# Kernel optimization log

Hardware: AMD Instinct MI355X
Metric: run time of the kernel (lower is better)

Reference implementation:

```python
import jax, jax.numpy as jnp
import numpy as np

K, D, E = 2048, 128, 64

def setup_inputs() -> dict:
    key = jax.random.key(0)
    k1, k2, k3 = jax.random.split(key, 3)
    z = jax.random.normal(k1, (K, D), dtype=jnp.float32)
    # Kaiming-like scaling so logits stay in a sane range
    W1 = jax.random.normal(k2, (2 * D, E), dtype=jnp.float32) / jnp.sqrt(2.0 * D)
    b1 = jnp.zeros((E,), dtype=jnp.float32)
    W2 = jax.random.normal(k3, (E, 1), dtype=jnp.float32) / jnp.sqrt(1.0 * E)
    b2 = jnp.zeros((1,), dtype=jnp.float32)
    return {"z": z, "W1": W1, "b1": b1, "W2": W2, "b2": b2}


def reference(z, W1, b1, W2, b2):
    # edge_mlp(cat([z_i, z_j])) == z_i @ W1[:d] + z_j @ W1[d:] + b1  (avoids (k,k,2d) concat)
    d = z.shape[1]
    hi = z @ W1[:d]          # (k, e)  -- contribution of z_i (row/query)
    hj = z @ W1[d:]          # (k, e)  -- contribution of z_j (col/key)
    h = jax.nn.silu(hi[:, None, :] + hj[None, :, :] + b1)   # (k, k, e)
    logits = jnp.einsum('ije,eo->ij', h, W2) + b2[0]         # (k, k)
    return jax.nn.softmax(logits, axis=-1)
```

## Files before the change

kernel.cpp:

```cpp
#include <hip/hip_runtime.h>
#include <cstdint>
#include <cstddef>

#define KTOT 2048
#define DDIM 128
#define EDIM 64
#define RPB  2
#define KPB  4

#define LOG2E 1.44269504088896f

typedef float v2f __attribute__((ext_vector_type(2)));

__global__ void proj_kernel(const float* __restrict__ z,
                            const float* __restrict__ W1,
                            const float* __restrict__ b1,
                            float* __restrict__ hi,
                            float* __restrict__ hj) {
  __shared__ float zrow[KPB][DDIM];
  const int t  = threadIdx.x;
  const int k0 = blockIdx.x * KPB;
#pragma unroll
  for (int r = 0; r < KPB; ++r) zrow[r][t] = z[(size_t)(k0 + r) * DDIM + t];
  __syncthreads();

  const int  e    = t & 63;
  const bool isHj = (t >= 64);
  const float* Wcol = W1 + (isHj ? DDIM * EDIM : 0) + e;

  float acc[KPB];
  const float binit = isHj ? 0.0f : b1[e];
#pragma unroll
  for (int r = 0; r < KPB; ++r) acc[r] = binit;

#pragma unroll 4
  for (int d = 0; d < DDIM; ++d) {
    const float w = Wcol[(size_t)d * EDIM];
#pragma unroll
    for (int r = 0; r < KPB; ++r) acc[r] = fmaf(zrow[r][d], w, acc[r]);
  }

  float* dst = isHj ? hj : hi;
#pragma unroll
  for (int r = 0; r < KPB; ++r)
    dst[(size_t)(k0 + r) * EDIM + e] = acc[r] * LOG2E;
}

__device__ __forceinline__ float quad_term(float4 hiq, float4 hvq, float4 w2q) {
  const v2f t01 = (v2f){hiq.x, hiq.y} + (v2f){hvq.x, hvq.y};
  const v2f t23 = (v2f){hiq.z, hiq.w} + (v2f){hvq.z, hvq.w};
  const float e0 = __builtin_amdgcn_exp2f(-t01.x);
  const float e1 = __builtin_amdgcn_exp2f(-t01.y);
  const float e2 = __builtin_amdgcn_exp2f(-t23.x);
  const float e3 = __builtin_amdgcn_exp2f(-t23.y);
  const v2f d01 = (v2f){e0, e1} + 1.0f;
  const v2f d23 = (v2f){e2, e3} + 1.0f;
  const v2f u01 = t01 * (v2f){w2q.x, w2q.y};
  const v2f u23 = t23 * (v2f){w2q.z, w2q.w};
  const float p01 = d01.x * d01.y;
  const float p23 = d23.x * d23.y;
  const float rD  = __builtin_amdgcn_rcpf(p01 * p23);
  const float n01 = fmaf(u01.y, d01.x, u01.x * d01.y);
  const float n23 = fmaf(u23.y, d23.x, u23.x * d23.y);
  const float N   = fmaf(n23, p01, n01 * p23);
  return N * rD;
}

__global__ __launch_bounds__(512, 8) void edge_softmax_kernel(
    const float* __restrict__ hi, const float* __restrict__ hj,
    const float* __restrict__ w2, float* __restrict__ out) {
  __shared__ float logits[RPB][KTOT];
  __shared__ float ps[RPB][4];

  const int tid  = threadIdx.x;
  const int lane = tid & 63;
  const int wave = tid >> 6;
  const int sub  = lane & 7;
  const int jg   = lane >> 3;
  const int i0   = blockIdx.x * RPB;

  const float4 w2a = *reinterpret_cast<const float4*>(w2 + sub * 8);
  const float4 w2b = *reinterpret_cast<const float4*>(w2 + sub * 8 + 4);
  float4 hia[RPB], hib[RPB];
#pragma unroll
  for (int r = 0; r < RPB; ++r) {
    hia[r] = *reinterpret_cast<const float4*>(hi + (size_t)(i0 + r) * EDIM + sub * 8);
    hib[r] = *reinterpret_cast<const float4*>(hi + (size_t)(i0 + r) * EDIM + sub * 8 + 4);
  }

  const int jbase = wave * 8 + jg;
  const float* hjp = hj + (size_t)jbase * EDIM + sub * 8;

  float4 hva = *reinterpret_cast<const float4*>(hjp);
  float4 hvb = *reinterpret_cast<const float4*>(hjp + 4);

  for (int it = 0; it < KTOT / 64; ++it) {
    const float4 ca = hva, cb = hvb;
    if (it + 1 < KTOT / 64) {
      const float* p = hjp + (size_t)(it + 1) * 64 * EDIM;
      hva = *reinterpret_cast<const float4*>(p);
      hvb = *reinterpret_cast<const float4*>(p + 4);
    }
    const int j = jbase + it * 64;
#pragma unroll
    for (int r = 0; r < RPB; ++r) {
      float a = quad_term(hia[r], ca, w2a) + quad_term(hib[r], cb, w2b);
      a += __shfl_xor(a, 1);
      a += __shfl_xor(a, 2);
      a += __shfl_xor(a, 4);
      if (sub == 0) logits[r][j] = a;
    }
  }
  __syncthreads();

  const int r = wave >> 2;
  const int q = wave & 3;
  float* lrow = logits[r];
  const int base = q * 512;

  float ssum = 0.0f;
#pragma unroll
  for (int t = 0; t < 8; ++t) {
    const int k = base + t * 64 + lane;
    const float ev = __builtin_amdgcn_exp2f(lrow[k]);
    lrow[k] = ev;
    ssum += ev;
  }
#pragma unroll
  for (int off = 32; off; off >>= 1) ssum += __shfl_xor(ssum, off);
  if (lane == 0) ps[r][q] = ssum;
  __syncthreads();
  ssum = ps[r][0] + ps[r][1] + ps[r][2] + ps[r][3];
  const float rinv = 1.0f / ssum;

  float* orow = out + (size_t)(i0 + r) * KTOT;
#pragma unroll
  for (int t = 0; t < 2; ++t) {
    const int k4 = q * 128 + t * 64 + lane;
    float4 v = *reinterpret_cast<const float4*>(&lrow[k4 * 4]);
    v.x *= rinv; v.y *= rinv; v.z *= rinv; v.w *= rinv;
    *reinterpret_cast<float4*>(&orow[k4 * 4]) = v;
  }
}

extern "C" void kernel_launch(void* const* d_in, const int* in_sizes, int n_in,
                              void* d_out, int out_size, void* d_ws, size_t ws_size,
                              hipStream_t stream) {
  const float* z  = (const float*)d_in[0];
  const float* W1 = (const float*)d_in[1];
  const float* b1 = (const float*)d_in[2];
  const float* W2 = (const float*)d_in[3];
  float* out = (float*)d_out;

  float* hi = (float*)d_ws;
  float* hj = hi + (size_t)KTOT * EDIM;

  hipLaunchKernelGGL(proj_kernel, dim3(KTOT / KPB), dim3(DDIM), 0, stream,
                     z, W1, b1, hi, hj);
  hipLaunchKernelGGL(edge_softmax_kernel, dim3(KTOT / RPB), dim3(512), 0, stream,
                     hi, hj, W2, out);
}
```

Baseline: 69.78 us.

## Factor sigmoid exponentials into per-node terms and process four rows per block

The change rewrites exp(-(hi+hj)) as exp(-hi)*exp(-hj), precomputing both exponentials and the w2-scaled projections in the projection kernel. This removes all transcendental exp calls from the K*K*E inner loop, leaving multiplies, adds and one reciprocal per group. The j-side loads are doubled (weighted term plus exponential), so RPB rises to 4 to amortize them over more rows, and launch bounds change to match. The risk is overflow or underflow in the product of exponentials for large logits, plus higher register pressure.

```diff
diff --git a/kernel.cpp b/kernel.cpp
--- a/kernel.cpp
+++ b/kernel.cpp
@@ -5,7 +5,7 @@
 #define KTOT 2048
 #define DDIM 128
 #define EDIM 64
-#define RPB  2
+#define RPB  4
 #define KPB  4
 
 #define LOG2E 1.44269504088896f
@@ -15,8 +15,9 @@
 __global__ void proj_kernel(const float* __restrict__ z,
                             const float* __restrict__ W1,
                             const float* __restrict__ b1,
-                            float* __restrict__ hi,
-                            float* __restrict__ hj) {
+                            const float* __restrict__ w2,
+                            float* __restrict__ hiw, float* __restrict__ Ei,
+                            float* __restrict__ hjw, float* __restrict__ Ej) {
   __shared__ float zrow[KPB][DDIM];
   const int t  = threadIdx.x;
   const int k0 = blockIdx.x * KPB;
@@ -40,37 +41,38 @@
     for (int r = 0; r < KPB; ++r) acc[r] = fmaf(zrow[r][d], w, acc[r]);
   }
 
-  float* dst = isHj ? hj : hi;
+  const float wv = w2[e];
+  float* dw = isHj ? hjw : hiw;
+  float* dE = isHj ? Ej  : Ei;
 #pragma unroll
-  for (int r = 0; r < KPB; ++r)
-    dst[(size_t)(k0 + r) * EDIM + e] = acc[r] * LOG2E;
+  for (int r = 0; r < KPB; ++r) {
+    const float tv = acc[r] * LOG2E;
+    dw[(size_t)(k0 + r) * EDIM + e] = tv * wv;
+    dE[(size_t)(k0 + r) * EDIM + e] = __builtin_amdgcn_exp2f(-tv);
+  }
 }
 
-__device__ __forceinline__ float quad_term(float4 hiq, float4 hvq, float4 w2q) {
-  const v2f t01 = (v2f){hiq.x, hiq.y} + (v2f){hvq.x, hvq.y};
-  const v2f t23 = (v2f){hiq.z, hiq.w} + (v2f){hvq.z, hvq.w};
-  const float e0 = __builtin_amdgcn_exp2f(-t01.x);
-  const float e1 = __builtin_amdgcn_exp2f(-t01.y);
-  const float e2 = __builtin_amdgcn_exp2f(-t23.x);
-  const float e3 = __builtin_amdgcn_exp2f(-t23.y);
-  const v2f d01 = (v2f){e0, e1} + 1.0f;
-  const v2f d23 = (v2f){e2, e3} + 1.0f;
-  const v2f u01 = t01 * (v2f){w2q.x, w2q.y};
-  const v2f u23 = t23 * (v2f){w2q.z, w2q.w};
+__device__ __forceinline__ void quad_nd(const float4 hw, const float4 he,
+                                        const float4 jw, const float4 je,
+                                        float& Nq, float& Dq) {
+  const v2f u01 = (v2f){hw.x, hw.y} + (v2f){jw.x, jw.y};
+  const v2f u23 = (v2f){hw.z, hw.w} + (v2f){jw.z, jw.w};
+  const v2f d01 = (v2f){he.x, he.y} * (v2f){je.x, je.y} + 1.0f;
+  const v2f d23 = (v2f){he.z, he.w} * (v2f){je.z, je.w} + 1.0f;
+  const float n01 = fmaf(u01.x, d01.y, u01.y * d01.x);
+  const float n23 = fmaf(u23.x, d23.y, u23.y * d23.x);
   const float p01 = d01.x * d01.y;
   const float p23 = d23.x * d23.y;
-  const float rD  = __builtin_amdgcn_rcpf(p01 * p23);
-  const float n01 = fmaf(u01.y, d01.x, u01.x * d01.y);
-  const float n23 = fmaf(u23.y, d23.x, u23.x * d23.y);
-  const float N   = fmaf(n23, p01, n01 * p23);
-  return N * rD;
+  Nq = fmaf(n01, p23, n23 * p01);
+  Dq = p01 * p23;
 }
 
-__global__ __launch_bounds__(512, 8) void edge_softmax_kernel(
-    const float* __restrict__ hi, const float* __restrict__ hj,
-    const float* __restrict__ w2, float* __restrict__ out) {
+__global__ __launch_bounds__(512, 4) void edge_softmax_kernel(
+    const float* __restrict__ hiw_, const float* __restrict__ Ei_,
+    const float* __restrict__ hjw_, const float* __restrict__ Ej_,
+    float* __restrict__ out) {
   __shared__ float logits[RPB][KTOT];
-  __shared__ float ps[RPB][4];
+  __shared__ float ps[RPB][2];
 
   const int tid  = threadIdx.x;
   const int lane = tid & 63;
@@ -79,32 +81,42 @@
   const int jg   = lane >> 3;
   const int i0   = blockIdx.x * RPB;
 
-  const float4 w2a = *reinterpret_cast<const float4*>(w2 + sub * 8);
-  const float4 w2b = *reinterpret_cast<const float4*>(w2 + sub * 8 + 4);
-  float4 hia[RPB], hib[RPB];
+  float4 hwA[RPB], hwB[RPB], heA[RPB], heB[RPB];
 #pragma unroll
   for (int r = 0; r < RPB; ++r) {
-    hia[r] = *reinterpret_cast<const float4*>(hi + (size_t)(i0 + r) * EDIM + sub * 8);
-    hib[r] = *reinterpret_cast<const float4*>(hi + (size_t)(i0 + r) * EDIM + sub * 8 + 4);
+    const size_t o = (size_t)(i0 + r) * EDIM + sub * 8;
+    hwA[r] = *reinterpret_cast<const float4*>(hiw_ + o);
+    hwB[r] = *reinterpret_cast<const float4*>(hiw_ + o + 4);
+    heA[r] = *reinterpret_cast<const float4*>(Ei_ + o);
+    heB[r] = *reinterpret_cast<const float4*>(Ei_ + o + 4);
   }
 
   const int jbase = wave * 8 + jg;
-  const float* hjp = hj + (size_t)jbase * EDIM + sub * 8;
+  const float* pjw = hjw_ + (size_t)jbase * EDIM + sub * 8;
+  const float* pje = Ej_  + (size_t)jbase * EDIM + sub * 8;
 
-  float4 hva = *reinterpret_cast<const float4*>(hjp);
-  float4 hvb = *reinterpret_cast<const float4*>(hjp + 4);
+  float4 jwA = *reinterpret_cast<const float4*>(pjw);
+  float4 jwB = *reinterpret_cast<const float4*>(pjw + 4);
+  float4 jeA = *reinterpret_cast<const float4*>(pje);
+  float4 jeB = *reinterpret_cast<const float4*>(pje + 4);
 
   for (int it = 0; it < KTOT / 64; ++it) {
-    const float4 ca = hva, cb = hvb;
+    const float4 cwA = jwA, cwB = jwB, ceA = jeA, ceB = jeB;
     if (it + 1 < KTOT / 64) {
-      const float* p = hjp + (size_t)(it + 1) * 64 * EDIM;
-      hva = *reinterpret_cast<const float4*>(p);
-      hvb = *reinterpret_cast<const float4*>(p + 4);
+      const size_t off = (size_t)(it + 1) * 64 * EDIM;
+      jwA = *reinterpret_cast<const float4*>(pjw + off);
+      jwB = *reinterpret_cast<const float4*>(pjw + off + 4);
+      jeA = *reinterpret_cast<const float4*>(pje + off);
+      jeB = *reinterpret_cast<const float4*>(pje + off + 4);
     }
     const int j = jbase + it * 64;
 #pragma unroll
     for (int r = 0; r < RPB; ++r) {
-      float a = quad_term(hia[r], ca, w2a) + quad_term(hib[r], cb, w2b);
+      float N0, D0, N1, D1;
+      quad_nd(hwA[r], heA[r], cwA, ceA, N0, D0);
+      quad_nd(hwB[r], heB[r], cwB, ceB, N1, D1);
+      const float rD = __builtin_amdgcn_rcpf(D0 * D1);
+      float a = fmaf(N0, D1, N1 * D0) * rD;
       a += __shfl_xor(a, 1);
       a += __shfl_xor(a, 2);
       a += __shfl_xor(a, 4);
@@ -113,14 +125,14 @@
   }
   __syncthreads();
 
-  const int r = wave >> 2;
-  const int q = wave & 3;
+  const int r = wave >> 1;
+  const int q = wave & 1;
   float* lrow = logits[r];
-  const int base = q * 512;
+  const int base = q * 1024;
 
   float ssum = 0.0f;
 #pragma unroll
-  for (int t = 0; t < 8; ++t) {
+  for (int t = 0; t < 16; ++t) {
     const int k = base + t * 64 + lane;
     const float ev = __builtin_amdgcn_exp2f(lrow[k]);
     lrow[k] = ev;
@@ -130,13 +142,12 @@
   for (int off = 32; off; off >>= 1) ssum += __shfl_xor(ssum, off);
   if (lane == 0) ps[r][q] = ssum;
   __syncthreads();
-  ssum = ps[r][0] + ps[r][1] + ps[r][2] + ps[r][3];
-  const float rinv = 1.0f / ssum;
+  const float rinv = 1.0f / (ps[r][0] + ps[r][1]);
 
   float* orow = out + (size_t)(i0 + r) * KTOT;
 #pragma unroll
-  for (int t = 0; t < 2; ++t) {
-    const int k4 = q * 128 + t * 64 + lane;
+  for (int t = 0; t < 4; ++t) {
+    const int k4 = q * 256 + t * 64 + lane;
     float4 v = *reinterpret_cast<const float4*>(&lrow[k4 * 4]);
     v.x *= rinv; v.y *= rinv; v.z *= rinv; v.w *= rinv;
     *reinterpret_cast<float4*>(&orow[k4 * 4]) = v;
@@ -152,11 +163,13 @@
   const float* W2 = (const float*)d_in[3];
   float* out = (float*)d_out;
 
-  float* hi = (float*)d_ws;
-  float* hj = hi + (size_t)KTOT * EDIM;
+  float* hiw = (float*)d_ws;
+  float* Ei  = hiw + (size_t)KTOT * EDIM;
+  float* hjw = Ei  + (size_t)KTOT * EDIM;
+  float* Ej  = hjw + (size_t)KTOT * EDIM;
 
   hipLaunchKernelGGL(proj_kernel, dim3(KTOT / KPB), dim3(DDIM), 0, stream,
-                     z, W1, b1, hi, hj);
+                     z, W1, b1, W2, hiw, Ei, hjw, Ej);
   hipLaunchKernelGGL(edge_softmax_kernel, dim3(KTOT / RPB), dim3(512), 0, stream,
-                     hi, hj, W2, out);
+                     hiw, Ei, hjw, Ej, out);
 }
```

Result: faster. 58.74 us (-15.8%).
